# Kernel optimization log

Measured on AMD Instinct MI355X. Metric: run time of the kernel, lower is better.

The kernel has to match this reference:

```python
import jax, jax.numpy as jnp
import numpy as np

N_LEVELS = 16
N_FEAT = 2
LOG2_T = 19
TABLE_SIZE = 1 << LOG2_T
COARSE = 16.0
FINE = 512.0
BOX_MIN = jnp.array([-1.0, -1.0, -1.0], jnp.float32)
BOX_MAX = jnp.array([1.0, 1.0, 1.0], jnp.float32)
# corner offsets, bit order (x, y, z) matching utils.BOX_OFFSETS / the trilinear code
OFFSETS = jnp.array([[0, 0, 0], [0, 0, 1], [0, 1, 0], [0, 1, 1],
                     [1, 0, 0], [1, 0, 1], [1, 1, 0], [1, 1, 1]], jnp.int32)
PRIMES = jnp.array([1, 2654435761, 805459861], dtype=jnp.uint32)
_b = np.exp((np.log(FINE) - np.log(COARSE)) / (N_LEVELS - 1))
RESOLUTIONS = jnp.asarray(np.floor(COARSE * _b ** np.arange(N_LEVELS)).astype(np.float32))


def setup_inputs() -> dict:
    key = jax.random.key(0)
    k1, k2 = jax.random.split(key)
    x = jax.random.uniform(k1, (1_000_000, 3), jnp.float32)  # inside the [-1,1]^3 box
    embeddings = jax.random.uniform(k2, (N_LEVELS, TABLE_SIZE, N_FEAT), jnp.float32,
                                    minval=-1e-4, maxval=1e-4)
    return {"x": x, "embeddings": embeddings}


def _hash(corners):
    # corners: (N, 8, 3) int32 -> (N, 8) int32 indices in [0, TABLE_SIZE)
    u = corners.astype(jnp.uint32) * PRIMES  # wraps mod 2^32, matching int32 wrap semantics
    h = u[..., 0] ^ u[..., 1] ^ u[..., 2]
    return (h & jnp.uint32(TABLE_SIZE - 1)).astype(jnp.int32)


def _level(x, table, res):
    grid = (BOX_MAX - BOX_MIN) / res                      # (3,)
    bl = jnp.floor((x - BOX_MIN) / grid).astype(jnp.int32)  # bottom-left voxel index (N,3)
    vmin = bl.astype(jnp.float32) * grid + BOX_MIN
    w = (x - vmin) / grid                                  # trilinear weights (N,3)
    idx = _hash(bl[:, None, :] + OFFSETS[None])            # (N,8)
    emb = table[idx]                                       # (N,8,F) gather
    # per-corner weight = prod over dims of (w if bit else 1-w) — same math as nested lerps
    cw = jnp.prod(jnp.where(OFFSETS[None].astype(bool), w[:, None, :], 1.0 - w[:, None, :]), axis=-1)
    return jnp.einsum('nk,nkf->nf', cw, emb)               # (N,F)


def reference(x, embeddings):
    x = jnp.clip(x, BOX_MIN, BOX_MAX)

    def body(_, lv):
        table, res = lv
        return None, _level(x, table, res)

    _, ys = jax.lax.scan(body, None, (embeddings, RESOLUTIONS))  # (L,N,F)
    return jnp.transpose(ys, (1, 0, 2)).reshape(x.shape[0], N_LEVELS * N_FEAT)
```

## Files before the change

kernel.cpp:

```cpp
#include <hip/hip_runtime.h>
#include <hip/hip_fp16.h>
#include <math.h>

#define N_LEVELS 16
#define LOG2_T 19
#define TABLE_SIZE (1 << LOG2_T)
#define IDX_MASK ((unsigned)(TABLE_SIZE - 1))
#define N_STAGED 4
#define N_FINE (N_LEVELS - N_STAGED)
#define DENSE_CAP 11936
#define N_LDS 2728
#define THREADS 256
#define ITERS 16
#define PTS_PER_BLOCK (32 * ITERS)

typedef float f2_t __attribute__((ext_vector_type(2)));
typedef float f4_t __attribute__((ext_vector_type(4)));

struct Params {
    float res[N_LEVELS];
    int   c0[N_STAGED];
    int   K[N_STAGED];
    int   K2[N_STAGED];
    int   base[N_STAGED + 1];
    int   n_pts;
};

__global__ __launch_bounds__(256) void convert_fine(
    const f2_t* __restrict__ emb, unsigned* __restrict__ tab, int n)
{
    int i = blockIdx.x * 256 + threadIdx.x;
    if (i >= n) return;
    f2_t e = __builtin_nontemporal_load(&emb[(size_t)N_STAGED * TABLE_SIZE + i]);
    union { __half2 h2; unsigned u; } c;
    c.h2 = __floats2half2_rn(e.x, e.y);
    __builtin_nontemporal_store(c.u, &tab[i]);
}

__global__ __launch_bounds__(256) void build_dense(
    const f2_t* __restrict__ emb, unsigned* __restrict__ dense, Params P)
{
    int t = blockIdx.x * 256 + threadIdx.x;
    if (t >= P.base[N_STAGED]) return;
    int lev = 3;
    if (t < P.base[3]) lev = 2;
    if (t < P.base[2]) lev = 1;
    if (t < P.base[1]) lev = 0;
    int li = t - P.base[lev];
    int K  = P.K[lev];
    if (li >= K * K * K) return;
    int kx = li % K; int r2 = li / K; int ky = r2 % K; int kz = r2 / K;
    unsigned cx = (unsigned)(P.c0[lev] + kx);
    unsigned cy = (unsigned)(P.c0[lev] + ky);
    unsigned cz = (unsigned)(P.c0[lev] + kz);
    unsigned h = (cx ^ (cy * 2654435761u) ^ (cz * 805459861u)) & IDX_MASK;
    f2_t e = emb[(size_t)lev * TABLE_SIZE + h];
    union { __half2 h2; unsigned u; } c;
    c.h2 = __floats2half2_rn(e.x, e.y);
    dense[t] = c.u;
}

__device__ __forceinline__ void acc_corner(
    unsigned w0, unsigned w1, float g0, float g1, float& a0, float& a1)
{
    union { unsigned u; __half2 h; } p0, p1;
    p0.u = w0; p1.u = w1;
    a0 += g0 * __low2float(p0.h)  + g1 * __low2float(p1.h);
    a1 += g0 * __high2float(p0.h) + g1 * __high2float(p1.h);
}

__device__ __forceinline__ unsigned pick4(uint4 g, unsigned s)
{
    unsigned t0 = (s & 1u) ? g.y : g.x;
    unsigned t1 = (s & 1u) ? g.w : g.z;
    return (s & 2u) ? t1 : t0;
}

#define GRID_SETUP(gridv)                                                  \
    float tx = (xx + 1.0f) / (gridv);                                      \
    float ty = (xy + 1.0f) / (gridv);                                      \
    float tz = (xz + 1.0f) / (gridv);                                      \
    int blx = (int)floorf(tx);                                             \
    int bly = (int)floorf(ty);                                             \
    int blz = (int)floorf(tz);                                             \
    float wx = (xx - ((float)blx * (gridv) + -1.0f)) / (gridv);            \
    float wy = (xy - ((float)bly * (gridv) + -1.0f)) / (gridv);            \
    float wz = (xz - ((float)blz * (gridv) + -1.0f)) / (gridv);            \
    float fy[2] = {1.0f - wy, wy};                                         \
    float fz[2] = {1.0f - wz, wz};                                         \
    float fx0 = 1.0f - wx, fx1 = wx;

__device__ __forceinline__ void eval_fine(
    float grid, const unsigned* __restrict__ tab,
    float xx, float xy, float xz, float& a0, float& a1)
{
    GRID_SETUP(grid)
    unsigned ux  = (unsigned)blx;
    unsigned hy0 = (unsigned)bly * 2654435761u;
    unsigned hy1 = ((unsigned)bly + 1u) * 2654435761u;
    unsigned hz0 = (unsigned)blz * 805459861u;
    unsigned hz1 = ((unsigned)blz + 1u) * 805459861u;
    unsigned w0a[4], w1a[4], i1a[4];
#pragma unroll
    for (int yz = 0; yz < 4; ++yz) {
        unsigned hyz = ((yz & 2) ? hy1 : hy0) ^ ((yz & 1) ? hz1 : hz0);
        unsigned i0 = (ux ^ hyz) & IDX_MASK;
        unsigned i1 = ((ux + 1u) ^ hyz) & IDX_MASK;
        i1a[yz] = i1;
        uint4 g = *(const uint4*)(tab + (i0 & ~3u));
        w0a[yz] = pick4(g, i0 & 3u);
        w1a[yz] = pick4(g, i1 & 3u);
    }
    if ((ux & 3u) == 3u) {
#pragma unroll
        for (int yz = 0; yz < 4; ++yz) w1a[yz] = tab[i1a[yz]];
    }
    a0 = 0.0f; a1 = 0.0f;
#pragma unroll
    for (int yz = 0; yz < 4; ++yz) {
        float wyz = fy[yz >> 1] * fz[yz & 1];
        acc_corner(w0a[yz], w1a[yz], fx0 * wyz, fx1 * wyz, a0, a1);
    }
}

template <int LEV, bool FROM_LDS>
__device__ __forceinline__ void eval_coarse(
    const Params& P, const unsigned* s_dense, const unsigned* __restrict__ denseG,
    const f2_t* __restrict__ emb,
    float xx, float xy, float xz, float& a0, float& a1)
{
    float grid = 2.0f / P.res[LEV];
    GRID_SETUP(grid)
    int K = P.K[LEV], K2 = P.K2[LEV];
    int kx = blx - P.c0[LEV], ky = bly - P.c0[LEV], kz = blz - P.c0[LEV];
    a0 = 0.0f; a1 = 0.0f;
    unsigned lim = (unsigned)(K - 1);
    if ((unsigned)kx < lim && (unsigned)ky < lim && (unsigned)kz < lim) {
        int i00 = (kz * K + ky) * K + kx;
        if (FROM_LDS) {
            int ib = P.base[LEV] + i00;
#pragma unroll
            for (int yz = 0; yz < 4; ++yz) {
                int id = ib + (yz >> 1) * K + (yz & 1) * K2;
                float wyz = fy[yz >> 1] * fz[yz & 1];
                acc_corner(s_dense[id], s_dense[id + 1], fx0 * wyz, fx1 * wyz,
                           a0, a1);
            }
        } else {
            const unsigned* tb = denseG + P.base[LEV];
#pragma unroll
            for (int yz = 0; yz < 4; ++yz) {
                unsigned id = (unsigned)(i00 + (yz >> 1) * K + (yz & 1) * K2);
                uint4 g = *(const uint4*)(tb + (id & ~3u));
                unsigned s0 = id & 3u;
                unsigned w0 = pick4(g, s0);
                unsigned w1;
                if (s0 == 3u) w1 = tb[id + 1u];
                else          w1 = pick4(g, s0 + 1u);
                float wyz = fy[yz >> 1] * fz[yz & 1];
                acc_corner(w0, w1, fx0 * wyz, fx1 * wyz, a0, a1);
            }
        }
    } else {
        const f2_t* tab = emb + (size_t)LEV * TABLE_SIZE;
#pragma unroll
        for (int k = 0; k < 8; ++k) {
            int bx = (k >> 2) & 1, by = (k >> 1) & 1, bz = k & 1;
            unsigned h = ((unsigned)(blx + bx)
                          ^ ((unsigned)(bly + by) * 2654435761u)
                          ^ ((unsigned)(blz + bz) * 805459861u)) & IDX_MASK;
            f2_t e = tab[h];
            float w = (bx ? wx : 1.0f - wx) * fy[by] * fz[bz];
            a0 += w * e.x; a1 += w * e.y;
        }
    }
}

__global__ __launch_bounds__(256) void ingp_hash_v5(
    const float* __restrict__ x,
    const unsigned* __restrict__ tabF,
    const unsigned* __restrict__ denseG,
    const f2_t* __restrict__ emb,
    float* __restrict__ out,
    Params P)
{
    __shared__ __align__(16) unsigned s_dense[N_LDS];
    __shared__ float s_res[N_LEVELS];
    {
        const uint4* src = (const uint4*)denseG;
        uint4* dst = (uint4*)s_dense;
        for (int id = threadIdx.x; id < N_LDS / 4; id += THREADS) dst[id] = src[id];
        if (threadIdx.x < N_LEVELS) s_res[threadIdx.x] = P.res[threadIdx.x];
    }
    __syncthreads();

    int lp  = threadIdx.x & 7;
    int ptl = threadIdx.x >> 3;

    float gridA = 2.0f / s_res[2 * lp];
    float gridB = 2.0f / s_res[2 * lp + 1];
    int fo = 2 * lp - 4; if (fo < 0) fo = 0;
    const unsigned* tA = tabF + (size_t)fo * TABLE_SIZE;
    const unsigned* tB = tabF + (size_t)(fo + 1) * TABLE_SIZE;

    int base_n = blockIdx.x * PTS_PER_BLOCK + ptl;

#pragma unroll 1
    for (int it = 0; it < ITERS; ++it) {
        int n = base_n + it * 32;
        int nc = n < P.n_pts ? n : P.n_pts - 1;
        float xx = fminf(fmaxf(__builtin_nontemporal_load(&x[nc * 3 + 0]), -1.0f), 1.0f);
        float xy = fminf(fmaxf(__builtin_nontemporal_load(&x[nc * 3 + 1]), -1.0f), 1.0f);
        float xz = fminf(fmaxf(__builtin_nontemporal_load(&x[nc * 3 + 2]), -1.0f), 1.0f);

        float r0, r1, r2, r3;
        if (lp == 0) {
            eval_coarse<0, true>(P, s_dense, denseG, emb, xx, xy, xz, r0, r1);
            eval_coarse<1, true>(P, s_dense, denseG, emb, xx, xy, xz, r2, r3);
        } else if (lp == 1) {
            eval_coarse<2, false>(P, s_dense, denseG, emb, xx, xy, xz, r0, r1);
            eval_coarse<3, false>(P, s_dense, denseG, emb, xx, xy, xz, r2, r3);
        } else {
            eval_fine(gridA, tA, xx, xy, xz, r0, r1);
            eval_fine(gridB, tB, xx, xy, xz, r2, r3);
        }

        if (n < P.n_pts) {
            f4_t o4 = {r0, r1, r2, r3};
            __builtin_nontemporal_store(
                o4, (f4_t*)(out + (size_t)n * (N_LEVELS * 2) + lp * 4));
        }
    }
}

__global__ __launch_bounds__(256) void ingp_hash_pair_f32(
    const float* __restrict__ x, const f2_t* __restrict__ emb,
    float* __restrict__ out, Params P)
{
    int b = blockIdx.x;
    int slot = b & 7;
    int n = (b >> 3) * 256 + (int)threadIdx.x;
    if (n >= P.n_pts) return;
    float xx = fminf(fmaxf(x[n * 3 + 0], -1.0f), 1.0f);
    float xy = fminf(fmaxf(x[n * 3 + 1], -1.0f), 1.0f);
    float xz = fminf(fmaxf(x[n * 3 + 2], -1.0f), 1.0f);
    float r0 = 0.f, r1 = 0.f, r2 = 0.f, r3 = 0.f;
#pragma unroll
    for (int hl = 0; hl < 2; ++hl) {
        int lev = 2 * slot + hl;
        float grid = 2.0f / P.res[lev];
        int blx = (int)floorf((xx + 1.0f) / grid);
        int bly = (int)floorf((xy + 1.0f) / grid);
        int blz = (int)floorf((xz + 1.0f) / grid);
        float wx = (xx - ((float)blx * grid + -1.0f)) / grid;
        float wy = (xy - ((float)bly * grid + -1.0f)) / grid;
        float wz = (xz - ((float)blz * grid + -1.0f)) / grid;
        const f2_t* tab = emb + (size_t)lev * TABLE_SIZE;
        float acc0 = 0.0f, acc1 = 0.0f;
#pragma unroll
        for (int k = 0; k < 8; ++k) {
            int bx = (k >> 2) & 1, by = (k >> 1) & 1, bz = k & 1;
            unsigned h = ((unsigned)(blx + bx)
                          ^ ((unsigned)(bly + by) * 2654435761u)
                          ^ ((unsigned)(blz + bz) * 805459861u)) & IDX_MASK;
            f2_t e = tab[h];
            float w = (bx ? wx : 1.0f - wx) * (by ? wy : 1.0f - wy) * (bz ? wz : 1.0f - wz);
            acc0 += w * e.x; acc1 += w * e.y;
        }
        if (hl == 0) { r0 = acc0; r1 = acc1; } else { r2 = acc0; r3 = acc1; }
    }
    f4_t o4 = {r0, r1, r2, r3};
    __builtin_nontemporal_store(o4, (f4_t*)(out + (size_t)n * (N_LEVELS * 2) + slot * 4));
}

extern "C" void kernel_launch(void* const* d_in, const int* in_sizes, int n_in,
                              void* d_out, int out_size, void* d_ws, size_t ws_size,
                              hipStream_t stream) {
    const float* x   = (const float*)d_in[0];
    const float* emb = (const float*)d_in[1];
    float* out = (float*)d_out;
    int n_pts = in_sizes[0] / 3;

    Params P;
    double b = exp((log(512.0) - log(16.0)) / 15.0);
    for (int i = 0; i < N_LEVELS; ++i)
        P.res[i] = (float)floor(16.0 * pow(b, (double)i));
    P.n_pts = n_pts;

    int base = 0;
    for (int l = 0; l < N_STAGED; ++l) {
        float grid = 2.0f / P.res[l];
        int blmin = (int)floorf(1.0f / grid);
        int blmax = (int)floorf(2.0f / grid);
        int K = blmax - blmin + 2;
        P.c0[l] = blmin; P.K[l] = K; P.K2[l] = K * K;
        P.base[l] = base;
        base += K * K * K;
        base = (base + 3) & ~3;
    }
    P.base[N_STAGED] = base;

    size_t need = (size_t)N_FINE * TABLE_SIZE * 4 + (size_t)DENSE_CAP * 4;
    bool ok = (base <= DENSE_CAP) && (P.base[2] == N_LDS) &&
              (ws_size >= need) && (d_ws != nullptr);
    if (ok) {
        unsigned* tabF   = (unsigned*)d_ws;
        unsigned* denseG = tabF + (size_t)N_FINE * TABLE_SIZE;
        int nF = N_FINE * TABLE_SIZE;
        hipLaunchKernelGGL(convert_fine, dim3((nF + 255) / 256), dim3(256), 0, stream,
                           (const f2_t*)emb, tabF, nF);
        hipLaunchKernelGGL(build_dense, dim3((base + 255) / 256), dim3(256), 0, stream,
                           (const f2_t*)emb, denseG, P);
        int blocks = (n_pts + PTS_PER_BLOCK - 1) / PTS_PER_BLOCK;
        hipLaunchKernelGGL(ingp_hash_v5, dim3(blocks), dim3(256), 0, stream,
                           x, tabF, denseG, (const f2_t*)emb, out, P);
    } else {
        int blocks = 8 * ((n_pts + 255) / 256);
        hipLaunchKernelGGL(ingp_hash_pair_f32, dim3(blocks), dim3(256), 0, stream,
                           x, (const f2_t*)emb, out, P);
    }
}
```

Measured before the change: 661.0 us.

## Switch to one-thread-per-point evaluating all levels, stage three dense levels in LDS

Replaces the 8-lanes-per-point split with a mapping where each thread evaluates all 16 levels for its own points. Level 3 now uses the hashed fp16 table instead of a global dense grid, so every level is converted to fp16. Levels 0-2 are staged densely in LDS. Hash gathers are issued as a batch before use to expose memory-level parallelism, and point coordinates are loaded with one vector read. The trade is higher per-thread register pressure and less lane-level gather coalescing, plus a larger LDS footprint that may lower occupancy.

```diff
diff --git a/kernel.cpp b/kernel.cpp
--- a/kernel.cpp
+++ b/kernel.cpp
@@ -6,13 +6,11 @@
 #define LOG2_T 19
 #define TABLE_SIZE (1 << LOG2_T)
 #define IDX_MASK ((unsigned)(TABLE_SIZE - 1))
-#define N_STAGED 4
-#define N_FINE (N_LEVELS - N_STAGED)
-#define DENSE_CAP 11936
-#define N_LDS 2728
+#define N_STAGED 3
+#define N_LDS 6104
 #define THREADS 256
-#define ITERS 16
-#define PTS_PER_BLOCK (32 * ITERS)
+#define PTS_PER_THREAD 2
+#define PTS_PER_BLOCK (THREADS * PTS_PER_THREAD)
 
 typedef float f2_t __attribute__((ext_vector_type(2)));
 typedef float f4_t __attribute__((ext_vector_type(4)));
@@ -26,12 +24,12 @@
     int   n_pts;
 };
 
-__global__ __launch_bounds__(256) void convert_fine(
+__global__ __launch_bounds__(256) void convert_all(
     const f2_t* __restrict__ emb, unsigned* __restrict__ tab, int n)
 {
     int i = blockIdx.x * 256 + threadIdx.x;
     if (i >= n) return;
-    f2_t e = __builtin_nontemporal_load(&emb[(size_t)N_STAGED * TABLE_SIZE + i]);
+    f2_t e = __builtin_nontemporal_load(&emb[i]);
     union { __half2 h2; unsigned u; } c;
     c.h2 = __floats2half2_rn(e.x, e.y);
     __builtin_nontemporal_store(c.u, &tab[i]);
@@ -42,8 +40,7 @@
 {
     int t = blockIdx.x * 256 + threadIdx.x;
     if (t >= P.base[N_STAGED]) return;
-    int lev = 3;
-    if (t < P.base[3]) lev = 2;
+    int lev = 2;
     if (t < P.base[2]) lev = 1;
     if (t < P.base[1]) lev = 0;
     int li = t - P.base[lev];
@@ -60,6 +57,13 @@
     dense[t] = c.u;
 }
 
+__device__ __forceinline__ unsigned pick4(uint4 g, unsigned s)
+{
+    unsigned t0 = (s & 1u) ? g.y : g.x;
+    unsigned t1 = (s & 1u) ? g.w : g.z;
+    return (s & 2u) ? t1 : t0;
+}
+
 __device__ __forceinline__ void acc_corner(
     unsigned w0, unsigned w1, float g0, float g1, float& a0, float& a1)
 {
@@ -67,13 +71,6 @@
     p0.u = w0; p1.u = w1;
     a0 += g0 * __low2float(p0.h)  + g1 * __low2float(p1.h);
     a1 += g0 * __high2float(p0.h) + g1 * __high2float(p1.h);
-}
-
-__device__ __forceinline__ unsigned pick4(uint4 g, unsigned s)
-{
-    unsigned t0 = (s & 1u) ? g.y : g.x;
-    unsigned t1 = (s & 1u) ? g.w : g.z;
-    return (s & 2u) ? t1 : t0;
 }
 
 #define GRID_SETUP(gridv)                                                  \
@@ -90,7 +87,7 @@
     float fz[2] = {1.0f - wz, wz};                                         \
     float fx0 = 1.0f - wx, fx1 = wx;
 
-__device__ __forceinline__ void eval_fine(
+__device__ __forceinline__ void eval_hash(
     float grid, const unsigned* __restrict__ tab,
     float xx, float xy, float xz, float& a0, float& a1)
 {
@@ -100,16 +97,21 @@
     unsigned hy1 = ((unsigned)bly + 1u) * 2654435761u;
     unsigned hz0 = (unsigned)blz * 805459861u;
     unsigned hz1 = ((unsigned)blz + 1u) * 805459861u;
-    unsigned w0a[4], w1a[4], i1a[4];
+    unsigned i0a[4], i1a[4];
 #pragma unroll
     for (int yz = 0; yz < 4; ++yz) {
         unsigned hyz = ((yz & 2) ? hy1 : hy0) ^ ((yz & 1) ? hz1 : hz0);
-        unsigned i0 = (ux ^ hyz) & IDX_MASK;
-        unsigned i1 = ((ux + 1u) ^ hyz) & IDX_MASK;
-        i1a[yz] = i1;
-        uint4 g = *(const uint4*)(tab + (i0 & ~3u));
-        w0a[yz] = pick4(g, i0 & 3u);
-        w1a[yz] = pick4(g, i1 & 3u);
+        i0a[yz] = (ux ^ hyz) & IDX_MASK;
+        i1a[yz] = ((ux + 1u) ^ hyz) & IDX_MASK;
+    }
+    uint4 g[4];
+#pragma unroll
+    for (int yz = 0; yz < 4; ++yz) g[yz] = *(const uint4*)(tab + (i0a[yz] & ~3u));
+    unsigned w0a[4], w1a[4];
+#pragma unroll
+    for (int yz = 0; yz < 4; ++yz) {
+        w0a[yz] = pick4(g[yz], i0a[yz] & 3u);
+        w1a[yz] = pick4(g[yz], i1a[yz] & 3u);
     }
     if ((ux & 3u) == 3u) {
 #pragma unroll
@@ -123,10 +125,9 @@
     }
 }
 
-template <int LEV, bool FROM_LDS>
-__device__ __forceinline__ void eval_coarse(
-    const Params& P, const unsigned* s_dense, const unsigned* __restrict__ denseG,
-    const f2_t* __restrict__ emb,
+template <int LEV>
+__device__ __forceinline__ void eval_lds(
+    const Params& P, const unsigned* s_dense, const f2_t* __restrict__ emb,
     float xx, float xy, float xz, float& a0, float& a1)
 {
     float grid = 2.0f / P.res[LEV];
@@ -136,30 +137,13 @@
     a0 = 0.0f; a1 = 0.0f;
     unsigned lim = (unsigned)(K - 1);
     if ((unsigned)kx < lim && (unsigned)ky < lim && (unsigned)kz < lim) {
-        int i00 = (kz * K + ky) * K + kx;
-        if (FROM_LDS) {
-            int ib = P.base[LEV] + i00;
-#pragma unroll
-            for (int yz = 0; yz < 4; ++yz) {
-                int id = ib + (yz >> 1) * K + (yz & 1) * K2;
-                float wyz = fy[yz >> 1] * fz[yz & 1];
-                acc_corner(s_dense[id], s_dense[id + 1], fx0 * wyz, fx1 * wyz,
-                           a0, a1);
-            }
-        } else {
-            const unsigned* tb = denseG + P.base[LEV];
-#pragma unroll
-            for (int yz = 0; yz < 4; ++yz) {
-                unsigned id = (unsigned)(i00 + (yz >> 1) * K + (yz & 1) * K2);
-                uint4 g = *(const uint4*)(tb + (id & ~3u));
-                unsigned s0 = id & 3u;
-                unsigned w0 = pick4(g, s0);
-                unsigned w1;
-                if (s0 == 3u) w1 = tb[id + 1u];
-                else          w1 = pick4(g, s0 + 1u);
-                float wyz = fy[yz >> 1] * fz[yz & 1];
-                acc_corner(w0, w1, fx0 * wyz, fx1 * wyz, a0, a1);
-            }
+        int ib = P.base[LEV] + (kz * K + ky) * K + kx;
+#pragma unroll
+        for (int yz = 0; yz < 4; ++yz) {
+            int id = ib + (yz >> 1) * K + (yz & 1) * K2;
+            float wyz = fy[yz >> 1] * fz[yz & 1];
+            acc_corner(s_dense[id], s_dense[id + 1], fx0 * wyz, fx1 * wyz,
+                       a0, a1);
         }
     } else {
         const f2_t* tab = emb + (size_t)LEV * TABLE_SIZE;
@@ -176,71 +160,75 @@
     }
 }
 
-__global__ __launch_bounds__(256) void ingp_hash_v5(
+__global__ __launch_bounds__(256) void ingp_hash_v8(
     const float* __restrict__ x,
-    const unsigned* __restrict__ tabF,
+    const unsigned* __restrict__ tabAll,
     const unsigned* __restrict__ denseG,
     const f2_t* __restrict__ emb,
     float* __restrict__ out,
     Params P)
 {
     __shared__ __align__(16) unsigned s_dense[N_LDS];
-    __shared__ float s_res[N_LEVELS];
     {
         const uint4* src = (const uint4*)denseG;
         uint4* dst = (uint4*)s_dense;
-        for (int id = threadIdx.x; id < N_LDS / 4; id += THREADS) dst[id] = src[id];
-        if (threadIdx.x < N_LEVELS) s_res[threadIdx.x] = P.res[threadIdx.x];
+        for (int id = threadIdx.x; id < N_LDS / 4; id += THREADS)
+            dst[id] = src[id];
     }
     __syncthreads();
 
-    int lp  = threadIdx.x & 7;
-    int ptl = threadIdx.x >> 3;
-
-    float gridA = 2.0f / s_res[2 * lp];
-    float gridB = 2.0f / s_res[2 * lp + 1];
-    int fo = 2 * lp - 4; if (fo < 0) fo = 0;
-    const unsigned* tA = tabF + (size_t)fo * TABLE_SIZE;
-    const unsigned* tB = tabF + (size_t)(fo + 1) * TABLE_SIZE;
-
-    int base_n = blockIdx.x * PTS_PER_BLOCK + ptl;
-
+    int base_pt = blockIdx.x * PTS_PER_BLOCK;
 #pragma unroll 1
-    for (int it = 0; it < ITERS; ++it) {
-        int n = base_n + it * 32;
-        int nc = n < P.n_pts ? n : P.n_pts - 1;
-        float xx = fminf(fmaxf(__builtin_nontemporal_load(&x[nc * 3 + 0]), -1.0f), 1.0f);
-        float xy = fminf(fmaxf(__builtin_nontemporal_load(&x[nc * 3 + 1]), -1.0f), 1.0f);
-        float xz = fminf(fmaxf(__builtin_nontemporal_load(&x[nc * 3 + 2]), -1.0f), 1.0f);
-
-        float r0, r1, r2, r3;
-        if (lp == 0) {
-            eval_coarse<0, true>(P, s_dense, denseG, emb, xx, xy, xz, r0, r1);
-            eval_coarse<1, true>(P, s_dense, denseG, emb, xx, xy, xz, r2, r3);
-        } else if (lp == 1) {
-            eval_coarse<2, false>(P, s_dense, denseG, emb, xx, xy, xz, r0, r1);
-            eval_coarse<3, false>(P, s_dense, denseG, emb, xx, xy, xz, r2, r3);
+    for (int j = 0; j < PTS_PER_THREAD; ++j) {
+        int n = base_pt + j * THREADS + (int)threadIdx.x;
+        if (n >= P.n_pts) continue;
+
+        float xx, xy, xz;
+        if (n < P.n_pts - 1) {
+            f4_t v;
+            __builtin_memcpy(&v, x + 3 * (size_t)n, 16);
+            xx = v.x; xy = v.y; xz = v.z;
         } else {
-            eval_fine(gridA, tA, xx, xy, xz, r0, r1);
-            eval_fine(gridB, tB, xx, xy, xz, r2, r3);
-        }
-
-        if (n < P.n_pts) {
-            f4_t o4 = {r0, r1, r2, r3};
-            __builtin_nontemporal_store(
-                o4, (f4_t*)(out + (size_t)n * (N_LEVELS * 2) + lp * 4));
+            xx = x[3 * (size_t)n]; xy = x[3 * (size_t)n + 1]; xz = x[3 * (size_t)n + 2];
+        }
+        xx = fminf(fmaxf(xx, -1.0f), 1.0f);
+        xy = fminf(fmaxf(xy, -1.0f), 1.0f);
+        xz = fminf(fmaxf(xz, -1.0f), 1.0f);
+
+        float* orow = out + (size_t)n * (N_LEVELS * 2);
+        float a0, a1, b0, b1;
+
+        eval_lds<0>(P, s_dense, emb, xx, xy, xz, a0, a1);
+        eval_lds<1>(P, s_dense, emb, xx, xy, xz, b0, b1);
+        { f4_t o = {a0, a1, b0, b1};
+          __builtin_nontemporal_store(o, (f4_t*)(orow + 0)); }
+
+        eval_lds<2>(P, s_dense, emb, xx, xy, xz, a0, a1);
+        eval_hash(2.0f / P.res[3], tabAll + (size_t)3 * TABLE_SIZE,
+                  xx, xy, xz, b0, b1);
+        { f4_t o = {a0, a1, b0, b1};
+          __builtin_nontemporal_store(o, (f4_t*)(orow + 4)); }
+
+#pragma unroll
+        for (int p = 2; p < 8; ++p) {
+            eval_hash(2.0f / P.res[2 * p], tabAll + (size_t)(2 * p) * TABLE_SIZE,
+                      xx, xy, xz, a0, a1);
+            eval_hash(2.0f / P.res[2 * p + 1], tabAll + (size_t)(2 * p + 1) * TABLE_SIZE,
+                      xx, xy, xz, b0, b1);
+            f4_t o = {a0, a1, b0, b1};
+            __builtin_nontemporal_store(o, (f4_t*)(orow + p * 4));
         }
     }
 }
 
 __global__ __launch_bounds__(256) void ingp_hash_pair_f32(
     const float* __restrict__ x, const f2_t* __restrict__ emb,
-    float* __restrict__ out, Params P)
+    float* __restrict__ out, int n_pts, Params P)
 {
     int b = blockIdx.x;
     int slot = b & 7;
     int n = (b >> 3) * 256 + (int)threadIdx.x;
-    if (n >= P.n_pts) return;
+    if (n >= n_pts) return;
     float xx = fminf(fmaxf(x[n * 3 + 0], -1.0f), 1.0f);
     float xy = fminf(fmaxf(x[n * 3 + 1], -1.0f), 1.0f);
     float xz = fminf(fmaxf(x[n * 3 + 2], -1.0f), 1.0f);
@@ -300,23 +288,22 @@
     }
     P.base[N_STAGED] = base;
 
-    size_t need = (size_t)N_FINE * TABLE_SIZE * 4 + (size_t)DENSE_CAP * 4;
-    bool ok = (base <= DENSE_CAP) && (P.base[2] == N_LDS) &&
-              (ws_size >= need) && (d_ws != nullptr);
+    size_t need = (size_t)N_LEVELS * TABLE_SIZE * 4 + (size_t)N_LDS * 4;
+    bool ok = (base == N_LDS) && (ws_size >= need) && (d_ws != nullptr);
     if (ok) {
-        unsigned* tabF   = (unsigned*)d_ws;
-        unsigned* denseG = tabF + (size_t)N_FINE * TABLE_SIZE;
-        int nF = N_FINE * TABLE_SIZE;
-        hipLaunchKernelGGL(convert_fine, dim3((nF + 255) / 256), dim3(256), 0, stream,
-                           (const f2_t*)emb, tabF, nF);
+        unsigned* tabAll = (unsigned*)d_ws;
+        unsigned* denseG = tabAll + (size_t)N_LEVELS * TABLE_SIZE;
+        int nAll = N_LEVELS * TABLE_SIZE;
+        hipLaunchKernelGGL(convert_all, dim3((nAll + 255) / 256), dim3(256), 0, stream,
+                           (const f2_t*)emb, tabAll, nAll);
         hipLaunchKernelGGL(build_dense, dim3((base + 255) / 256), dim3(256), 0, stream,
                            (const f2_t*)emb, denseG, P);
         int blocks = (n_pts + PTS_PER_BLOCK - 1) / PTS_PER_BLOCK;
-        hipLaunchKernelGGL(ingp_hash_v5, dim3(blocks), dim3(256), 0, stream,
-                           x, tabF, denseG, (const f2_t*)emb, out, P);
+        hipLaunchKernelGGL(ingp_hash_v8, dim3(blocks), dim3(256), 0, stream,
+                           x, tabAll, denseG, (const f2_t*)emb, out, P);
     } else {
         int blocks = 8 * ((n_pts + 255) / 256);
         hipLaunchKernelGGL(ingp_hash_pair_f32, dim3(blocks), dim3(256), 0, stream,
-                           x, (const f2_t*)emb, out, P);
-    }
-}
+                           x, (const f2_t*)emb, out, n_pts, P);
+    }
+}
```

After: 603.9 us. -8.6%, faster.
